# Kernel tuning notes

Hardware: AMD Instinct MI355X
Metric: run time of the kernel (lower is better)

Reference implementation:

```python
import jax, jax.numpy as jnp
import numpy as np

V = 50257
VPAD = 50304
D = 768
H = 6
HD = 128
L = 12
T = 2048
BLOCK = 128
NB = T // BLOCK
EPS = 1.1920929e-07  # torch.finfo(float32).eps, F.rms_norm default
ATTN_SCALE = 0.12


def rms_norm(x):
    return x * jax.lax.rsqrt(jnp.mean(jnp.square(x), axis=-1, keepdims=True) + EPS)


def rotary_tables(t):
    af = (1.0 / 1024) ** jnp.linspace(0.0, 1.0, HD // 4)
    af = jnp.concatenate([af, jnp.zeros(HD // 4)])  # half of HD/2 freqs are zero
    theta = jnp.arange(t, dtype=jnp.float32)[:, None] * af[None, :]  # [T, HD/2]
    return jnp.cos(theta), jnp.sin(theta)


def apply_rotary(x, cos, sin):
    # x: [B,T,H,HD]
    x1, x2 = jnp.split(x, 2, axis=-1)
    c = cos[None, :, None, :]
    s = sin[None, :, None, :]
    return jnp.concatenate([x1 * c + x2 * s, -x1 * s + x2 * c], axis=-1)


def build_elem_masks(input_seq, sw_long):
    # Reproduces create_block_masks: block-sparse document-causal + sliding window.
    docs = jnp.cumsum((input_seq == 50256).astype(jnp.int32))
    bi = jnp.arange(NB)
    docs_b = docs.reshape(NB, BLOCK)
    dlo, dhi = docs_b[:, 0], docs_b[:, -1]
    any_bm = (bi[:, None] >= bi[None, :]) & (dlo[:, None] <= dhi[None, :]) & (dhi[:, None] >= dlo[None, :])
    all_bm = (bi[:, None] > bi[None, :]) & (dlo[:, None] == dhi[None, :]) & (dhi[:, None] == dlo[None, :])
    partial_bm = any_bm & (~all_bm)

    def rank_desc(m):
        # rank of each True block among that row's True blocks ordered by descending kv index
        mi = m.astype(jnp.int32)
        return jnp.cumsum(mi[:, ::-1], axis=1)[:, ::-1] - mi

    pr = rank_desc(partial_bm)
    fr = rank_desc(all_bm)
    full_cnt = jnp.sum(all_bm.astype(jnp.int32), axis=1)
    ti = jnp.arange(T)
    causal_e = ti[:, None] >= ti[None, :]
    doc_e = docs[:, None] == docs[None, :]

    def bm(sw):
        # BlockMask.from_kv_blocks keeps nearest blocks:
        # partial kept count = min(partial_cnt, max(sw - full_cnt, 1)); full kept count = min(full_cnt, sw - 1)
        keep_p = partial_bm & (pr < jnp.maximum(sw - full_cnt, 1)[:, None])
        keep_f = all_bm & (fr < (sw - 1))
        kp = jnp.repeat(jnp.repeat(keep_p, BLOCK, axis=0), BLOCK, axis=1)
        kf = jnp.repeat(jnp.repeat(keep_f, BLOCK, axis=0), BLOCK, axis=1)
        # full blocks skip mask_mod; partial blocks apply elementwise document_causal
        return kf | (kp & causal_e & doc_e)

    return bm(sw_long), bm(sw_long // 2)


def attention(x, ve, qkv_w, lam, proj_w, cos, sin, mask):
    B = x.shape[0]
    qkv = jnp.einsum('btd,fd->btf', x, qkv_w.reshape(3 * H * HD, D))
    q, k, v = [a.reshape(B, T, H, HD) for a in jnp.split(qkv, 3, axis=-1)]
    q = apply_rotary(rms_norm(q), cos, sin)
    k = apply_rotary(rms_norm(k), cos, sin)
    if ve is not None:
        v = lam[0] * v + lam[1] * ve.reshape(v.shape)
    else:
        v = lam[0] * v
    scores = jnp.einsum('bthd,bshd->bhts', q, k) * ATTN_SCALE
    scores = jnp.where(mask[None, None], scores, -jnp.inf)
    p = jax.nn.softmax(scores, axis=-1)
    y = jnp.einsum('bhts,bshd->bthd', p, v).reshape(B, T, H * HD)
    return y @ proj_w.T


def mlp(x, fc_w, proj_w):
    h = x @ fc_w.T
    return jnp.square(jax.nn.relu(h)) @ proj_w.T


def forward(input_seq, target_seq, sw, embed_w, ve_w, qkv_w, attn_lambdas, attn_proj_w,
            mlp_fc_w, mlp_proj_w, block_lambdas, skip_weights, lm_head_w):
    long_m, short_m = build_elem_masks(input_seq, sw)
    cos, sin = rotary_tables(T)
    x = x0 = rms_norm(embed_w[input_seq][None])  # [1,T,D]
    ve0, ve1, ve2 = ve_w[0][input_seq], ve_w[1][input_seq], ve_w[2][input_seq]
    ve = [ve0, ve1, ve2, None, None, None, None, None, None, ve0, ve1, ve2]
    enc_masks = [long_m, short_m, short_m, short_m, long_m, short_m]
    masks = enc_masks + enc_masks[::-1]
    skips = []
    for i in range(6):  # encoder
        x = block_lambdas[i, 0] * x + block_lambdas[i, 1] * x0
        x = x + attention(rms_norm(x), ve[i], qkv_w[i], attn_lambdas[i], attn_proj_w[i], cos, sin, masks[i])
        x = x + mlp(rms_norm(x), mlp_fc_w[i], mlp_proj_w[i])
        skips.append(x)
    for j in range(6):  # decoder with U-net skips
        i = 6 + j
        x = x + skip_weights[j] * skips.pop()
        x = block_lambdas[i, 0] * x + block_lambdas[i, 1] * x0
        if i != 7:  # layer 7 has no attention
            x = x + attention(rms_norm(x), ve[i], qkv_w[i], attn_lambdas[i], attn_proj_w[i], cos, sin, masks[i])
        x = x + mlp(rms_norm(x), mlp_fc_w[i], mlp_proj_w[i])
    x = rms_norm(x)
    logits = (x @ lm_head_w.T).astype(jnp.float32)
    logits = 30.0 * jax.nn.sigmoid(logits / (7.5 * (D ** 0.5)))
    logp = jax.nn.log_softmax(logits.reshape(T, VPAD), axis=-1)
    return -jnp.mean(jnp.take_along_axis(logp, target_seq[:, None], axis=1))


def setup_inputs():
    key = jax.random.key(0)
    ks = jax.random.split(key, 10)

    def rn(k, shape, std):
        return jax.random.normal(k, shape, dtype=jnp.float32) * std

    s_d = 0.5 / (D ** 0.5)
    s_h = 0.5 / ((4 * D) ** 0.5)
    input_seq = jax.random.randint(ks[0], (T,), 0, V)
    input_seq = input_seq.at[jnp.arange(0, T, 512)].set(50256)  # doc separators
    return {
        'input_seq': input_seq,
        'target_seq': jax.random.randint(ks[1], (T,), 0, V),
        'sliding_window_num_blocks': 8,
        'embed_w': rn(ks[2], (V, D), 0.02),
        've_w': rn(ks[3], (3, V, D), 0.02),
        'qkv_w': rn(ks[4], (L, 3, H * HD, D), s_d),
        'attn_lambdas': jnp.tile(jnp.array([0.5, 0.5], dtype=jnp.float32), (L, 1)),
        'attn_proj_w': rn(ks[5], (L, D, H * HD), s_d),
        'mlp_fc_w': rn(ks[6], (L, 4 * D, D), s_d),
        'mlp_proj_w': rn(ks[7], (L, D, 4 * D), s_h),
        'block_lambdas': jnp.tile(jnp.array([1.0, 0.0], dtype=jnp.float32), (L, 1)),
        'skip_weights': jnp.ones((6,), dtype=jnp.float32),
        'lm_head_w': rn(ks[8], (VPAD, D), 0.005),
    }


def reference(input_seq, target_seq, sliding_window_num_blocks, embed_w, ve_w, qkv_w,
              attn_lambdas, attn_proj_w, mlp_fc_w, mlp_proj_w, block_lambdas,
              skip_weights, lm_head_w):
    return forward(input_seq, target_seq, sliding_window_num_blocks, embed_w, ve_w, qkv_w,
                   attn_lambdas, attn_proj_w, mlp_fc_w, mlp_proj_w, block_lambdas,
                   skip_weights, lm_head_w)
```

## Files before the change

### kernel.cpp

```cpp
#include <hip/hip_runtime.h>
#include <hip/hip_bf16.h>

#define TT 2048
#define DD 768
#define HH 6
#define HDIM 128
#define NL 12
#define NBL 16
#define BLKSZ 128
#define DFF 3072
#define VP 50304
#define NV 50257
#define EPSF 1.1920929e-07f

typedef unsigned short u16;
typedef __attribute__((ext_vector_type(8))) short short8v;
typedef __attribute__((ext_vector_type(4))) float f32x4;
typedef __attribute__((address_space(3))) void lds_void;
typedef __attribute__((address_space(1))) void gbl_void;

__device__ __forceinline__ u16 f2bf(float f){
  unsigned u = __float_as_uint(f);
  return (u16)((u + 0x7fffu + ((u >> 16) & 1u)) >> 16);
}
__device__ __forceinline__ float bf2f(u16 u){
  return __uint_as_float((unsigned)u << 16);
}
__device__ __forceinline__ void async16(const void* g, void* l){
  __builtin_amdgcn_global_load_lds((const gbl_void*)g, (lds_void*)l, 16, 0, 0);
}

__device__ __forceinline__ float wave_sum(float v){
#pragma unroll
  for (int o = 32; o > 0; o >>= 1) v += __shfl_xor(v, o);
  return v;
}
__device__ __forceinline__ float block_sum(float v){
  __shared__ float sh[9];
  int lane = threadIdx.x & 63, w = threadIdx.x >> 6;
  v = wave_sum(v);
  if (lane == 0) sh[w] = v;
  __syncthreads();
  if (threadIdx.x == 0){
    float tot = 0.f;
    int nw = (blockDim.x + 63) >> 6;
    for (int i = 0; i < nw; i++) tot += sh[i];
    sh[8] = tot;
  }
  __syncthreads();
  return sh[8];
}

__global__ void k_f2bf_all(const float* __restrict__ qkvw, const float* __restrict__ aproj,
                           const float* __restrict__ fcw, const float* __restrict__ mproj,
                           const float* __restrict__ lmw,
                           u16* __restrict__ qkvw_bf, u16* __restrict__ aprojw_bf,
                           u16* __restrict__ fcw_bf, u16* __restrict__ mprojw_bf,
                           u16* __restrict__ lmw_bf){
  const long S0 = 2654208;
  const long S1 = S0 + 884736;
  const long S2 = S1 + 3538944;
  const long S3 = S2 + 3538944;
  const long S4 = S3 + 4829184;
  long stride = (long)gridDim.x * blockDim.x;
  for (long g = (long)blockIdx.x * blockDim.x + threadIdx.x; g < S4; g += stride){
    const float* in; u16* out; long off;
    if (g < S0){ in = qkvw;  out = qkvw_bf;  off = g; }
    else if (g < S1){ in = aproj; out = aprojw_bf; off = g - S0; }
    else if (g < S2){ in = fcw;   out = fcw_bf;   off = g - S1; }
    else if (g < S3){ in = mproj; out = mprojw_bf; off = g - S2; }
    else { in = lmw; out = lmw_bf; off = g - S3; }
    const float4* p = (const float4*)(in + off * 8);
    float4 a = p[0], b = p[1];
    u16 o[8] = { f2bf(a.x), f2bf(a.y), f2bf(a.z), f2bf(a.w),
                 f2bf(b.x), f2bf(b.y), f2bf(b.z), f2bf(b.w) };
    *(ulonglong2*)(out + off * 8) = *(const ulonglong2*)o;
  }
}

__global__ void k_docs_masks(const int* __restrict__ seq, const int* __restrict__ swnb,
                             int* __restrict__ docs, int* __restrict__ bmask){
  int lane = threadIdx.x;
  int cnt = 0;
  for (int i = 0; i < 32; i++) cnt += (seq[lane*32 + i] == 50256);
  int incl = cnt;
#pragma unroll
  for (int o = 1; o < 64; o <<= 1){
    int v = __shfl_up(incl, o);
    if (lane >= o) incl += v;
  }
  int run = incl - cnt;
  for (int i = 0; i < 32; i++){
    int t = lane*32 + i;
    run += (seq[t] == 50256);
    docs[t] = run;
  }
  __syncthreads();
  if (lane != 0) return;
  int dlo[NBL], dhi[NBL];
  for (int b = 0; b < NBL; b++){ dlo[b] = docs[b*BLKSZ]; dhi[b] = docs[b*BLKSZ + BLKSZ-1]; }
  int allb[NBL][NBL], partb[NBL][NBL];
  for (int i = 0; i < NBL; i++)
    for (int j = 0; j < NBL; j++){
      int a = (i >= j) && (dlo[i] <= dhi[j]) && (dhi[i] >= dlo[j]);
      int f = (i >  j) && (dlo[i] == dhi[j]) && (dhi[i] == dlo[j]);
      allb[i][j] = f; partb[i][j] = a && !f;
    }
  int sws[2]; sws[0] = swnb[0]; sws[1] = swnb[0] / 2;
  for (int m = 0; m < 2; m++){
    int sw = sws[m];
    for (int i = 0; i < NBL; i++){
      int fullcnt = 0;
      for (int j = 0; j < NBL; j++) fullcnt += allb[i][j];
      int pth = sw - fullcnt; if (pth < 1) pth = 1;
      int pr = 0, fr = 0;
      for (int j = NBL-1; j >= 0; j--){
        int kp = partb[i][j] && (pr < pth);
        int kf = allb[i][j]  && (fr < sw - 1);
        bmask[(m*2+0)*NBL*NBL + i*NBL + j] = kf;
        bmask[(m*2+1)*NBL*NBL + i*NBL + j] = kp;
        pr += partb[i][j]; fr += allb[i][j];
      }
    }
  }
}

__global__ void k_embed(const int* __restrict__ seq, const float* __restrict__ embw,
                        const float* __restrict__ vew, float* __restrict__ x,
                        float* __restrict__ x0, u16* __restrict__ veg,
                        float* __restrict__ cosb, float* __restrict__ sinb){
  int t = blockIdx.x;
  if (threadIdx.x < 64){
    int j = threadIdx.x;
    float c = 1.f, s = 0.f;
    if (j < 32){
      float af = powf(1.0f/1024.0f, (float)j / 31.0f);
      float th = (float)t * af;
      c = cosf(th); s = sinf(th);
    }
    cosb[t*64 + j] = c; sinb[t*64 + j] = s;
  }
  int tok = seq[t];
  const float* row = embw + (size_t)tok * DD;
  float ss = 0.f;
  for (int d = threadIdx.x; d < DD; d += blockDim.x){ float v = row[d]; ss += v*v; }
  float tot = block_sum(ss);
  float rn = rsqrtf(tot / DD + EPSF);
  for (int d = threadIdx.x; d < DD; d += blockDim.x){
    float v = row[d] * rn;
    x[(size_t)t*DD + d] = v; x0[(size_t)t*DD + d] = v;
  }
  for (int j = 0; j < 3; j++){
    const float* vr = vew + ((size_t)j*NV + tok) * DD;
    u16* dst = veg + ((size_t)j*TT + t) * DD;
    for (int d = threadIdx.x; d < DD; d += blockDim.x) dst[d] = f2bf(vr[d]);
  }
}

__global__ void k_rmsnorm_bf(const float* __restrict__ in, u16* __restrict__ out,
                             float* __restrict__ rowsum){
  int t = blockIdx.x;
  if (rowsum && threadIdx.x == 0) rowsum[t] = 0.f;
  const float* r = in + (size_t)t * DD;
  float ss = 0.f;
  for (int d = threadIdx.x; d < DD; d += blockDim.x){ float v = r[d]; ss += v*v; }
  float tot = block_sum(ss);
  float rn = rsqrtf(tot / DD + EPSF);
  u16* o = out + (size_t)t * DD;
  for (int d = threadIdx.x; d < DD; d += blockDim.x) o[d] = f2bf(r[d] * rn);
}

__global__ void k_premix_norm(float* __restrict__ x, const float* __restrict__ x0,
                              const float* __restrict__ sk, float* __restrict__ sk_out,
                              const float* __restrict__ skw, int j,
                              const float* __restrict__ bl, int layer, u16* __restrict__ xn){
  int t = blockIdx.x;
  float bl0 = bl[layer*2], bl1 = bl[layer*2 + 1];
  float sw = sk ? skw[j] : 0.f;
  float vloc[3];
  float ss = 0.f;
  int base = t * DD;
#pragma unroll
  for (int k = 0; k < 3; k++){
    int d = threadIdx.x + k*256;
    float xin = x[base + d];
    if (sk_out) sk_out[base + d] = xin;
    float v = xin;
    if (sk) v += sw * sk[base + d];
    v = bl0 * v + bl1 * x0[base + d];
    vloc[k] = v; ss += v*v;
  }
  float tot = block_sum(ss);
  float rn = rsqrtf(tot / DD + EPSF);
#pragma unroll
  for (int k = 0; k < 3; k++){
    int d = threadIdx.x + k*256;
    x[base + d] = vloc[k];
    xn[base + d] = f2bf(vloc[k] * rn);
  }
}

template<int MODE, int BN>
__global__ __launch_bounds__(256, (BN == 64) ? 4 : 2)
void k_mfma_gemm(const u16* __restrict__ A, const u16* __restrict__ B,
                 float* __restrict__ C, u16* __restrict__ Cbf,
                 const u16* __restrict__ vegp, const float* __restrict__ lam,
                 int layer, u16* __restrict__ vtb,
                 const float* __restrict__ cosb, const float* __restrict__ sinb,
                 u16* __restrict__ qbf, u16* __restrict__ kbf,
                 int N, int K, int ldk, int nbn){
  constexpr int NW  = BN / 32;
  constexpr int BC  = BN / 64 * 2;
  __shared__ u16 As[128*64];
  __shared__ u16 Bs[BN*64];
  __shared__ float qt[(MODE == 4) ? 32*132 : 1];
  int per = (nbn << 4) >> 3;
  int x = (blockIdx.x & 7) * per + (blockIdx.x >> 3);
  int bm = (x & 15) << 7;
  int bn = (x >> 4) * BN;
  int koff = (MODE == 5) ? blockIdx.y * K : 0;
  int tid = threadIdx.x;
  int wid = tid >> 6, lane = tid & 63;
  int wr = wid >> 1, wc = wid & 1;
  int srow = lane >> 3;
  int scol = (((lane & 7) ^ srow) * 8);
  int l15 = lane & 15, l16 = lane >> 4;
  const u16* pa[4];
  const u16* pb[BC];
#pragma unroll
  for (int c = 0; c < 4; c++){
    int row = (wid*4 + c)*8 + srow;
    pa[c] = A + (size_t)(bm + row) * ldk + koff + scol;
  }
#pragma unroll
  for (int c = 0; c < BC; c++){
    int row = (wid*BC + c)*8 + srow;
    pb[c] = B + (size_t)(bn + row) * ldk + koff + scol;
  }
  f32x4 acc[4][NW] = {};
  for (int k0 = 0; k0 < K; k0 += 64){
#pragma unroll
    for (int c = 0; c < 4; c++){
      async16(pa[c], As + (wid*4 + c) * 512);
      pa[c] += 64;
    }
#pragma unroll
    for (int c = 0; c < BC; c++){
      async16(pb[c], Bs + (wid*BC + c) * 512);
      pb[c] += 64;
    }
    __syncthreads();
#pragma unroll
    for (int kk = 0; kk < 2; kk++){
      short8v a[4], b[NW];
#pragma unroll
      for (int m = 0; m < 4; m++){
        int row = wr*64 + m*16 + l15;
        a[m] = *(const short8v*)(As + row*64 + ((((kk<<2)|l16) ^ (row&7))<<3));
      }
#pragma unroll
      for (int n = 0; n < NW; n++){
        int row = wc*(BN/2) + n*16 + l15;
        b[n] = *(const short8v*)(Bs + row*64 + ((((kk<<2)|l16) ^ (row&7))<<3));
      }
#pragma unroll
      for (int m = 0; m < 4; m++)
#pragma unroll
        for (int n = 0; n < NW; n++)
          acc[m][n] = __builtin_amdgcn_mfma_f32_16x16x32_bf16(a[m], b[n], acc[m][n], 0, 0, 0);
    }
    __syncthreads();
  }
  if (MODE == 4){
    if (bn >= 1536){
      int h = (bn - 1536) >> 7;
      float l0 = lam[layer*2], l1 = lam[layer*2 + 1];
#pragma unroll
      for (int m = 0; m < 4; m++){
        int t0 = bm + wr*64 + m*16 + l16*4;
#pragma unroll
        for (int n = 0; n < NW; n++){
          int d = wc*64 + n*16 + l15;
          u16 o[4];
#pragma unroll
          for (int j = 0; j < 4; j++){
            float v = l0 * acc[m][n][j];
            if (vegp) v += l1 * bf2f(vegp[(size_t)(t0 + j)*DD + h*HDIM + d]);
            o[j] = f2bf(v);
          }
          *(ushort4*)(vtb + ((size_t)(h*HDIM + d))*TT + t0) = *(const ushort4*)o;
        }
      }
    } else {
      int h = (bn < 768) ? (bn >> 7) : ((bn - 768) >> 7);
      u16* dstb = (bn < 768) ? qbf : kbf;
#pragma unroll
      for (int p = 0; p < 4; p++){
        if (wr == (p >> 1)){
#pragma unroll
          for (int mm = 0; mm < 2; mm++){
            int m = (p & 1)*2 + mm;
#pragma unroll
            for (int n = 0; n < NW; n++){
              int col = wc*64 + n*16 + l15;
#pragma unroll
              for (int j = 0; j < 4; j++){
                int lr = m*16 + l16*4 + j - (p & 1)*32;
                qt[lr*132 + col] = acc[m][n][j];
              }
            }
          }
        }
        __syncthreads();
        {
          int row = tid >> 3, part = tid & 7;
          int tok = bm + p*32 + row;
          float ss = 0.f;
#pragma unroll
          for (int jj = 0; jj < 16; jj++){
            float v = qt[row*132 + part*16 + jj];
            ss += v*v;
          }
          ss += __shfl_xor(ss, 1); ss += __shfl_xor(ss, 2); ss += __shfl_xor(ss, 4);
          float rn = rsqrtf(ss / 128.f + EPSF);
          if (part < 4){
            u16* dst = dstb + ((size_t)(h*TT + tok))*HDIM;
#pragma unroll
            for (int jj = 0; jj < 16; jj++){
              int j = part*16 + jj;
              float c = cosb[tok*64 + j], s = sinb[tok*64 + j];
              float v1 = qt[row*132 + j] * rn;
              float v2 = qt[row*132 + j + 64] * rn;
              dst[j]      = f2bf(v1*c + v2*s);
              dst[j + 64] = f2bf(-v1*s + v2*c);
            }
          }
        }
        __syncthreads();
      }
    }
    return;
  }
#pragma unroll
  for (int m = 0; m < 4; m++){
    int row = bm + wr*64 + m*16 + l16*4;
#pragma unroll
    for (int j = 0; j < 4; j++){
      if (MODE == 3){
        u16* cb = Cbf + (size_t)(row + j) * N + bn + wc*(BN/2) + l15;
#pragma unroll
        for (int n = 0; n < NW; n++){
          float v = fmaxf(acc[m][n][j], 0.f);
          cb[n*16] = f2bf(v * v);
        }
      } else if (MODE == 5){
        float* cp = C + (size_t)(row + j) * N + bn + wc*(BN/2) + l15;
#pragma unroll
        for (int n = 0; n < NW; n++) atomicAdd(cp + n*16, acc[m][n][j]);
      } else {
        float* cp = C + (size_t)(row + j) * N + bn + wc*(BN/2) + l15;
#pragma unroll
        for (int n = 0; n < NW; n++) cp[n*16] = acc[m][n][j];
      }
    }
  }
}

__global__ __launch_bounds__(256) void k_loss_mfma(const u16* __restrict__ A, const u16* __restrict__ B,
                                                   const int* __restrict__ tgt, float* __restrict__ rowsum,
                                                   float* __restrict__ tl){
  __shared__ u16 As[128*64];
  __shared__ u16 Bs[128*64];
  const int nbn = VP/128;
  int per = (nbn << 4) >> 3;
  int x = (blockIdx.x & 7) * per + (blockIdx.x >> 3);
  int bm = (x & 15) << 7;
  int bn = (x >> 4) << 7;
  int tid = threadIdx.x;
  int wid = tid >> 6, lane = tid & 63;
  int wr = wid >> 1, wc = wid & 1;
  int srow = lane >> 3;
  int scol = (((lane & 7) ^ srow) * 8);
  int l15 = lane & 15, l16 = lane >> 4;
  const u16* pa[4];
  const u16* pb[4];
#pragma unroll
  for (int c = 0; c < 4; c++){
    int row = (wid*4 + c)*8 + srow;
    pa[c] = A + (size_t)(bm + row) * DD + scol;
    pb[c] = B + (size_t)(bn + row) * DD + scol;
  }
  f32x4 acc[4][4] = {};
  for (int k0 = 0; k0 < DD; k0 += 64){
#pragma unroll
    for (int c = 0; c < 4; c++){
      int chunk = wid * 4 + c;
      async16(pa[c], As + chunk * 512);
      async16(pb[c], Bs + chunk * 512);
      pa[c] += 64; pb[c] += 64;
    }
    __syncthreads();
#pragma unroll
    for (int kk = 0; kk < 2; kk++){
      short8v a[4], b[4];
#pragma unroll
      for (int m = 0; m < 4; m++)
        a[m] = *(const short8v*)(As + (wr*64 + m*16 + l15)*64 + ((((kk<<2)|l16) ^ (l15&7))<<3));
#pragma unroll
      for (int n = 0; n < 4; n++)
        b[n] = *(const short8v*)(Bs + (wc*64 + n*16 + l15)*64 + ((((kk<<2)|l16) ^ (l15&7))<<3));
#pragma unroll
      for (int m = 0; m < 4; m++)
#pragma unroll
        for (int n = 0; n < 4; n++)
          acc[m][n] = __builtin_amdgcn_mfma_f32_16x16x32_bf16(a[m], b[n], acc[m][n], 0, 0, 0);
    }
    __syncthreads();
  }
  const float INVS = 0.0048112522432469f;
#pragma unroll
  for (int m = 0; m < 4; m++){
#pragma unroll
    for (int j = 0; j < 4; j++){
      int row = bm + wr*64 + m*16 + l16*4 + j;
      int tg = tgt[row];
      float rs = 0.f;
#pragma unroll
      for (int n = 0; n < 4; n++){
        int col = bn + wc*64 + n*16 + l15;
        float lg = 30.f / (1.f + __expf(-acc[m][n][j] * INVS));
        rs += __expf(lg);
        if (col == tg) tl[row] = lg;
      }
      rs += __shfl_xor(rs, 1); rs += __shfl_xor(rs, 2);
      rs += __shfl_xor(rs, 4); rs += __shfl_xor(rs, 8);
      if (l15 == 0) atomicAdd(&rowsum[row], rs);
    }
  }
}

__global__ __launch_bounds__(256) void k_attn_mfma(
    const u16* __restrict__ qbf, const u16* __restrict__ kbf, const u16* __restrict__ vtb,
    u16* __restrict__ y, const int* __restrict__ docs,
    const int* __restrict__ kfm, const int* __restrict__ kpm){
  __shared__ u16 Ks[128*128];
  __shared__ u16 Vs[128*128];
  __shared__ int docsL[128];
  __shared__ int kb[NBL], kfl[NBL];
  __shared__ int nkb_sh;
  int wg = (blockIdx.x & 7) * 24 + (blockIdx.x >> 3);
  int h = wg >> 5;
  int qb = (31 - (wg & 31)) * 64;
  int bt = qb >> 7;
  int tid = threadIdx.x;
  int w = tid >> 6, lane = tid & 63;
  int l15 = lane & 15, l16 = lane >> 4;
  if (tid == 0){
    int n = 0;
    for (int sb = 0; sb <= bt; sb++){
      int kf = kfm[bt*NBL + sb], kp = kpm[bt*NBL + sb];
      if (kf || kp){ kb[n] = sb; kfl[n] = kf; n++; }
    }
    nkb_sh = n;
  }
  short8v q[4];
  {
    const u16* qrow = qbf + ((size_t)(h*TT + qb + w*16 + l15))*HDIM;
#pragma unroll
    for (int kc = 0; kc < 4; kc++) q[kc] = *(const short8v*)(qrow + kc*32 + l16*8);
  }
  int t_row[4], dq[4];
#pragma unroll
  for (int j = 0; j < 4; j++){
    t_row[j] = qb + w*16 + l16*4 + j;
    dq[j] = docs[t_row[j]];
  }
  f32x4 o[8] = {};
  float m[4], l[4];
#pragma unroll
  for (int j = 0; j < 4; j++){ m[j] = -1e30f; l[j] = 0.f; }
  __syncthreads();
  int nkb = nkb_sh;
  for (int bi = 0; bi < nkb; bi++){
    int kbi = kb[bi], kf = kfl[bi];
    __syncthreads();
    {
      const u16* ksrc = kbf + ((size_t)(h*TT + kbi*128))*HDIM;
      const u16* vsrc = vtb + ((size_t)(h*HDIM))*TT + kbi*128;
#pragma unroll
      for (int p = 0; p < 8; p++){
        int idx = tid + p*256;
        int r = idx >> 4, c = (idx & 15) * 8;
        short8v kv = *(const short8v*)(ksrc + (size_t)r*HDIM + c);
        *(short8v*)(Ks + ((r*128 + c) ^ ((r&7)<<3))) = kv;
        short8v vv = *(const short8v*)(vsrc + (size_t)r*TT + c);
        *(short8v*)(Vs + ((r*128 + c) ^ ((r&7)<<3))) = vv;
      }
      if (tid < 32) ((int4*)docsL)[tid] = ((const int4*)(docs + kbi*128))[tid];
    }
    __syncthreads();
    f32x4 s[8];
#pragma unroll
    for (int n = 0; n < 8; n++){
      f32x4 acc = {};
#pragma unroll
      for (int kc = 0; kc < 4; kc++){
        int row = n*16 + l15;
        short8v b = *(const short8v*)(Ks + ((row*128 + kc*32 + l16*8) ^ ((row&7)<<3)));
        acc = __builtin_amdgcn_mfma_f32_16x16x32_bf16(q[kc], b, acc, 0, 0, 0);
      }
      s[n] = acc;
    }
    int sbase = kbi*128;
    float bmax[4];
#pragma unroll
    for (int j = 0; j < 4; j++) bmax[j] = -1e30f;
#pragma unroll
    for (int n = 0; n < 8; n++){
      int sg = sbase + n*16 + l15;
      int ds = docsL[n*16 + l15];
#pragma unroll
      for (int j = 0; j < 4; j++){
        float sv = s[n][j] * 0.12f;
        bool keep = kf || ((sg <= t_row[j]) && (ds == dq[j]));
        sv = keep ? sv : -1e30f;
        s[n][j] = sv;
        bmax[j] = fmaxf(bmax[j], sv);
      }
    }
#pragma unroll
    for (int j = 0; j < 4; j++){
#pragma unroll
      for (int off = 1; off < 16; off <<= 1) bmax[j] = fmaxf(bmax[j], __shfl_xor(bmax[j], off));
      float nm = fmaxf(m[j], bmax[j]);
      float r = __expf(m[j] - nm);
      m[j] = nm; l[j] *= r;
#pragma unroll
      for (int n = 0; n < 8; n++) o[n][j] *= r;
    }
    __syncthreads();
#pragma unroll
    for (int n = 0; n < 8; n++){
#pragma unroll
      for (int j = 0; j < 4; j++){
        float sv = s[n][j];
        float p = (sv > -1e29f) ? __expf(sv - m[j]) : 0.f;
        l[j] += p;
        int prow = w*16 + l16*4 + j;
        Ks[((prow*128) + n*16 + l15) ^ ((prow&7)<<3)] = f2bf(p);
      }
    }
    __syncthreads();
    short8v a[4];
    {
      int prow = w*16 + l15;
#pragma unroll
      for (int kc = 0; kc < 4; kc++)
        a[kc] = *(const short8v*)(Ks + ((prow*128 + kc*32 + l16*8) ^ ((prow&7)<<3)));
    }
#pragma unroll
    for (int n = 0; n < 8; n++){
#pragma unroll
      for (int kc = 0; kc < 4; kc++){
        int vrow = n*16 + l15;
        short8v b = *(const short8v*)(Vs + ((vrow*128 + kc*32 + l16*8) ^ ((vrow&7)<<3)));
        o[n] = __builtin_amdgcn_mfma_f32_16x16x32_bf16(a[kc], b, o[n], 0, 0, 0);
      }
    }
  }
  float inv[4];
#pragma unroll
  for (int j = 0; j < 4; j++){
    float lt = l[j];
#pragma unroll
    for (int off = 1; off < 16; off <<= 1) lt += __shfl_xor(lt, off);
    inv[j] = 1.f / lt;
  }
#pragma unroll
  for (int n = 0; n < 8; n++){
#pragma unroll
    for (int j = 0; j < 4; j++)
      y[(size_t)t_row[j]*DD + h*HDIM + n*16 + l15] = f2bf(o[n][j] * inv[j]);
  }
}

__global__ void k_loss_final(const float* __restrict__ rowsum, const float* __restrict__ tl,
                             float* __restrict__ out){
  float a = 0.f;
  for (int t = threadIdx.x; t < TT; t += 256) a += logf(rowsum[t]) - tl[t];
  a = block_sum(a);
  if (threadIdx.x == 0) out[0] = a / TT;
}

extern "C" void kernel_launch(void* const* d_in, const int* in_sizes, int n_in,
                              void* d_out, int out_size, void* d_ws, size_t ws_size,
                              hipStream_t stream){
  const int*   seq   = (const int*)d_in[0];
  const int*   tgt   = (const int*)d_in[1];
  const int*   swnb  = (const int*)d_in[2];
  const float* embw  = (const float*)d_in[3];
  const float* vew   = (const float*)d_in[4];
  const float* qkvw  = (const float*)d_in[5];
  const float* alam  = (const float*)d_in[6];
  const float* aproj = (const float*)d_in[7];
  const float* fcw   = (const float*)d_in[8];
  const float* mproj = (const float*)d_in[9];
  const float* blam  = (const float*)d_in[10];
  const float* skw   = (const float*)d_in[11];
  const float* lmw   = (const float*)d_in[12];

  char* base = (char*)d_ws;
  size_t off = 0;
  auto alloc = [&](size_t bytes){ char* p = base + off; off += (bytes + 255) & ~(size_t)255; return p; };
  float* x     = (float*)alloc((size_t)TT*DD*4);
  float* x0    = (float*)alloc((size_t)TT*DD*4);
  float* skips = (float*)alloc((size_t)5*TT*DD*4);
  float* cosb  = (float*)alloc((size_t)TT*64*4);
  float* sinb  = (float*)alloc((size_t)TT*64*4);
  float* rowsum= (float*)alloc(TT*4);
  float* tl    = (float*)alloc(TT*4);
  int* docs    = (int*)alloc(TT*4);
  int* bmask   = (int*)alloc(4*NBL*NBL*4);
  u16* veg     = (u16*)alloc((size_t)3*TT*DD*2);
  u16* xn_bf   = (u16*)alloc((size_t)TT*DD*2);
  u16* y_bf    = (u16*)alloc((size_t)TT*DD*2);
  u16* hb_bf   = (u16*)alloc((size_t)TT*DFF*2);
  u16* qbf     = (u16*)alloc((size_t)HH*TT*HDIM*2);
  u16* kbf     = (u16*)alloc((size_t)HH*TT*HDIM*2);
  u16* vtb     = (u16*)alloc((size_t)HH*HDIM*TT*2);
  u16* qkvw_bf = (u16*)alloc((size_t)NL*2304*DD*2);
  u16* aprojw_bf = (u16*)alloc((size_t)NL*DD*DD*2);
  u16* fcw_bf  = (u16*)alloc((size_t)NL*DFF*DD*2);
  u16* mprojw_bf = (u16*)alloc((size_t)NL*DD*DFF*2);
  u16* lmw_bf  = (u16*)alloc((size_t)VP*DD*2);

  k_f2bf_all<<<4096, 256, 0, stream>>>(qkvw, aproj, fcw, mproj, lmw,
                                       qkvw_bf, aprojw_bf, fcw_bf, mprojw_bf, lmw_bf);
  k_docs_masks<<<1, 64, 0, stream>>>(seq, swnb, docs, bmask);
  k_embed<<<TT, 256, 0, stream>>>(seq, embw, vew, x, x0, veg, cosb, sinb);

  static const int msel[12] = {0,1,1,1,0,1, 1,0,1,1,1,0};
  for (int i = 0; i < NL; i++){
    const float* sk = nullptr;
    if (i == 6) sk = x;
    else if (i > 6) sk = skips + (size_t)(11 - i)*TT*DD;
    float* sk_out = (i >= 1 && i <= 5) ? (skips + (size_t)(i - 1)*TT*DD) : nullptr;
    k_premix_norm<<<TT, 256, 0, stream>>>(x, x0, sk, sk_out, skw, i - 6, blam, i, xn_bf);
    if (i != 7){
      const u16* vp = nullptr;
      if (i < 3) vp = veg + (size_t)i*TT*DD;
      else if (i >= 9) vp = veg + (size_t)(i - 9)*TT*DD;
      k_mfma_gemm<4,128><<<16*18, 256, 0, stream>>>(xn_bf, qkvw_bf + (size_t)i*2304*DD, nullptr,
                                                    nullptr, vp, alam, i, vtb, cosb, sinb, qbf, kbf,
                                                    2304, DD, DD, 18);
      const int* kfm = bmask + (msel[i]*2 + 0)*NBL*NBL;
      const int* kpm = bmask + (msel[i]*2 + 1)*NBL*NBL;
      k_attn_mfma<<<192, 256, 0, stream>>>(qbf, kbf, vtb, y_bf, docs, kfm, kpm);
      dim3 gap(16*12, 2);
      k_mfma_gemm<5,64><<<gap, 256, 0, stream>>>(y_bf, aprojw_bf + (size_t)i*DD*DD, x,
                                                 nullptr, nullptr, nullptr, 0, nullptr,
                                                 nullptr, nullptr, nullptr, nullptr, DD, 384, DD, 12);
      k_rmsnorm_bf<<<TT, 256, 0, stream>>>(x, xn_bf, nullptr);
    }
    k_mfma_gemm<3,64><<<16*48, 256, 0, stream>>>(xn_bf, fcw_bf + (size_t)i*DFF*DD, nullptr,
                                                 hb_bf, nullptr, nullptr, 0, nullptr,
                                                 nullptr, nullptr, nullptr, nullptr, DFF, DD, DD, 48);
    dim3 gmp(16*12, 4);
    k_mfma_gemm<5,64><<<gmp, 256, 0, stream>>>(hb_bf, mprojw_bf + (size_t)i*DD*DFF, x,
                                               nullptr, nullptr, nullptr, 0, nullptr,
                                               nullptr, nullptr, nullptr, nullptr, DD, 768, DFF, 12);
  }
  k_rmsnorm_bf<<<TT, 256, 0, stream>>>(x, xn_bf, rowsum);
  k_loss_mfma<<<16*(VP/128), 256, 0, stream>>>(xn_bf, lmw_bf, tgt, rowsum, tl);
  k_loss_final<<<1, 256, 0, stream>>>(rowsum, tl, (float*)d_out);
}
```

Measured before the change: 2.179 ms.

## Double-buffer LDS tiles in BN=64 GEMM to overlap global loads with MFMA

New measurement: 2.163 ms. About the same (-0.7%).

```diff
diff --git a/kernel.cpp b/kernel.cpp
--- a/kernel.cpp
+++ b/kernel.cpp
@@ -201,7 +201,7 @@
 }
 
 template<int MODE, int BN>
-__global__ __launch_bounds__(256, (BN == 64) ? 4 : 2)
+__global__ __launch_bounds__(256, (BN == 64) ? 3 : 2)
 void k_mfma_gemm(const u16* __restrict__ A, const u16* __restrict__ B,
                  float* __restrict__ C, u16* __restrict__ Cbf,
                  const u16* __restrict__ vegp, const float* __restrict__ lam,
@@ -209,10 +209,11 @@
                  const float* __restrict__ cosb, const float* __restrict__ sinb,
                  u16* __restrict__ qbf, u16* __restrict__ kbf,
                  int N, int K, int ldk, int nbn){
-  constexpr int NW  = BN / 32;
-  constexpr int BC  = BN / 64 * 2;
-  __shared__ u16 As[128*64];
-  __shared__ u16 Bs[BN*64];
+  constexpr int NW   = BN / 32;
+  constexpr int BC   = BN / 32;
+  constexpr int NBUF = (BN == 64) ? 2 : 1;
+  __shared__ u16 As[NBUF][128*64];
+  __shared__ u16 Bs[NBUF][BN*64];
   __shared__ float qt[(MODE == 4) ? 32*132 : 1];
   int per = (nbn << 4) >> 3;
   int x = (blockIdx.x & 7) * per + (blockIdx.x >> 3);
@@ -238,30 +239,31 @@
     pb[c] = B + (size_t)(bn + row) * ldk + koff + scol;
   }
   f32x4 acc[4][NW] = {};
-  for (int k0 = 0; k0 < K; k0 += 64){
+  auto stage = [&](int buf){
 #pragma unroll
     for (int c = 0; c < 4; c++){
-      async16(pa[c], As + (wid*4 + c) * 512);
+      async16(pa[c], &As[buf][(wid*4 + c) * 512]);
       pa[c] += 64;
     }
 #pragma unroll
     for (int c = 0; c < BC; c++){
-      async16(pb[c], Bs + (wid*BC + c) * 512);
+      async16(pb[c], &Bs[buf][(wid*BC + c) * 512]);
       pb[c] += 64;
     }
-    __syncthreads();
+  };
+  auto compute = [&](int buf){
 #pragma unroll
     for (int kk = 0; kk < 2; kk++){
       short8v a[4], b[NW];
 #pragma unroll
       for (int m = 0; m < 4; m++){
         int row = wr*64 + m*16 + l15;
-        a[m] = *(const short8v*)(As + row*64 + ((((kk<<2)|l16) ^ (row&7))<<3));
+        a[m] = *(const short8v*)(&As[buf][row*64 + ((((kk<<2)|l16) ^ (row&7))<<3)]);
       }
 #pragma unroll
       for (int n = 0; n < NW; n++){
         int row = wc*(BN/2) + n*16 + l15;
-        b[n] = *(const short8v*)(Bs + row*64 + ((((kk<<2)|l16) ^ (row&7))<<3));
+        b[n] = *(const short8v*)(&Bs[buf][row*64 + ((((kk<<2)|l16) ^ (row&7))<<3)]);
       }
 #pragma unroll
       for (int m = 0; m < 4; m++)
@@ -269,7 +271,31 @@
         for (int n = 0; n < NW; n++)
           acc[m][n] = __builtin_amdgcn_mfma_f32_16x16x32_bf16(a[m], b[n], acc[m][n], 0, 0, 0);
     }
-    __syncthreads();
+  };
+  if constexpr (BN == 64){
+    stage(0);
+    int KT = K >> 6;
+    for (int t = 0; t < KT; t++){
+      int cur = t & 1;
+      if (t + 1 < KT){
+        stage(cur ^ 1);
+        asm volatile("s_waitcnt vmcnt(6)" ::: "memory");
+      } else {
+        asm volatile("s_waitcnt vmcnt(0)" ::: "memory");
+      }
+      __builtin_amdgcn_s_barrier();
+      asm volatile("" ::: "memory");
+      compute(cur);
+      asm volatile("" ::: "memory");
+      __builtin_amdgcn_s_barrier();
+    }
+  } else {
+    for (int k0 = 0; k0 < K; k0 += 64){
+      stage(0);
+      __syncthreads();
+      compute(0);
+      __syncthreads();
+    }
   }
   if (MODE == 4){
     if (bn >= 1536){
@@ -428,7 +454,7 @@
 #pragma unroll
       for (int n = 0; n < 4; n++){
         int col = bn + wc*64 + n*16 + l15;
-        float lg = 30.f / (1.f + __expf(-acc[m][n][j] * INVS));
+        float lg = 30.f * __builtin_amdgcn_rcpf(1.f + __expf(-acc[m][n][j] * INVS));
         rs += __expf(lg);
         if (col == tg) tl[row] = lg;
       }
```
